# Performance work log

Hardware: AMD Instinct MI355X
Metric: run time of the kernel (lower is better)

## Reference

```python
import jax, jax.numpy as jnp
import numpy as np

REEIG_EPS = 1e-4  # SPDNet ReEig eigenvalue floor


def _semi_orth(key, ni, no):
    a = jax.random.normal(key, (ni, no), dtype=jnp.float32)
    q, _ = jnp.linalg.qr(a)  # columns orthonormal (ni >= no)
    return q[None]  # (1, ni, no)


def setup_inputs() -> dict:
    key = jax.random.key(0)
    ks = jax.random.split(key, 6)
    N, C, T, V = 256, 256, 64, 25
    x = jax.random.normal(ks[0], (N, C, T, V), dtype=jnp.float32)
    W1 = _semi_orth(ks[1], 25, 20)
    W2 = _semi_orth(ks[2], 20, 15)
    W3 = _semi_orth(ks[3], 15, 10)
    fc_w = jax.random.normal(ks[4], (64, 100), dtype=jnp.float32) * (1.0 / np.sqrt(100))
    fc_b = jax.random.normal(ks[5], (64,), dtype=jnp.float32) * 0.01
    return {"x": x, "W1": W1, "W2": W2, "W3": W3, "fc_w": fc_w, "fc_b": fc_b}


def _bimap(X, W):
    # X: (n, h, ni, ni), W: (h, ni, no) -> W^T X W : (n, h, no, no)
    return jnp.einsum('hji,nhjk,hkl->nhil', W, X, W)


def _reeig(X):
    w, u = jnp.linalg.eigh(X)
    w = jnp.maximum(w, REEIG_EPS)
    return jnp.einsum('...ij,...j,...kj->...ik', u, w, u)


def _logeig(X):
    w, u = jnp.linalg.eigh(X)
    return jnp.einsum('...ij,...j,...kj->...ik', u, jnp.log(w), u)


def reference(x, W1, W2, W3, fc_w, fc_b):
    N, C, T, V = x.shape
    xm = x.mean(axis=2)                      # (N, C, V): mean over time
    d = xm - xm.mean(axis=1, keepdims=True)  # center over channel samples
    cov = jnp.einsum('ncv,ncw->nvw', d, d) / (C - 1)  # (N, V, V), fused reduction
    cov = cov + jnp.float32(1e-8) * jnp.eye(V, dtype=x.dtype)
    X = cov[:, None, :, :]                   # (N, 1, V, V)
    X = _reeig(_bimap(X, W1))                # 25 -> 20
    X = _reeig(_bimap(X, W2))                # 20 -> 15
    X = _logeig(_reeig(_bimap(X, W3)))       # 15 -> 10, matrix log
    feat = X.reshape(N, -1)                  # (N, 100)
    return feat @ fc_w.T + fc_b              # (N, 64)
```

## Files before the change

### kernel.cpp

```cpp
#include <hip/hip_runtime.h>
#include <math.h>


__device__ __constant__ int d_pairs[9][5][2] = {
    {{9,0},{1,8},{2,7},{3,6},{4,5}},
    {{9,1},{2,0},{3,8},{4,7},{5,6}},
    {{9,2},{3,1},{4,0},{5,8},{6,7}},
    {{9,3},{4,2},{5,1},{6,0},{7,8}},
    {{9,4},{5,3},{6,2},{7,1},{8,0}},
    {{9,5},{6,4},{7,3},{8,2},{0,1}},
    {{9,6},{7,5},{8,4},{0,3},{1,2}},
    {{9,7},{8,6},{0,5},{1,4},{2,3}},
    {{9,8},{0,7},{1,6},{2,5},{3,4}},
};

__global__ __launch_bounds__(256) void topo_kernel(
    const float* __restrict__ x,
    const float* __restrict__ W1,
    const float* __restrict__ W2,
    const float* __restrict__ W3,
    const float* __restrict__ fcw,
    const float* __restrict__ fcb,
    float* __restrict__ out)
{
    __shared__ float s_xm[6400];
    __shared__ float s_mean[32];
    __shared__ float s_w1[500];
    __shared__ float s_w2[300];
    __shared__ float s_w3[152];
    __shared__ float s_t1[375];
    __shared__ float s_wc[250];
    __shared__ float s_E[2560];
    __shared__ float s_A[100];
    __shared__ float s_U[100];
    __shared__ float s_cp[10], s_cq[10];
    __shared__ int   s_ip[10], s_iq[10];
    __shared__ float s_lw[16];
    __shared__ float s_Y[100];
    __shared__ float s_fcw[100 * 65];

    const int tid = threadIdx.x;
    const int n = blockIdx.x;
    const float* xb = x + (size_t)n * (256 * 64 * 25);

    for (int g = tid; g < 6400; g += 256) {
        int o = g / 100, k = g - o * 100;
        s_fcw[k * 65 + o] = fcw[g];
    }
    for (int g = tid; g < 500; g += 256) s_w1[g] = W1[g];
    for (int g = tid; g < 300; g += 256) s_w2[g] = W2[g];
    if (tid < 150) s_w3[tid] = W3[tid];

    float acc[25];
    int   bidx[25];
#pragma unroll
    for (int k = 0; k < 25; ++k) {
        int o = tid + 256 * k;
        int c = o / 25, v = o - c * 25;
        bidx[k] = c * 1600 + v;
        acc[k] = 0.0f;
    }
#pragma unroll 4
    for (int t = 0; t < 64; ++t) {
#pragma unroll
        for (int k = 0; k < 25; ++k) {
            acc[k] += __builtin_nontemporal_load(&xb[bidx[k] + t * 25]);
        }
    }
#pragma unroll
    for (int k = 0; k < 25; ++k)
        s_xm[tid + 256 * k] = acc[k] * (1.0f / 64.0f);
    __syncthreads();

    for (int g = tid; g < 375; g += 256) {
        int i = g / 15, l = g - i * 15;
        float s = 0.0f;
#pragma unroll
        for (int j = 0; j < 20; ++j) s += s_w1[i * 20 + j] * s_w2[j * 15 + l];
        s_t1[g] = s;
    }
    if (tid < 25) {
        float s = 0.0f;
        for (int c = 0; c < 256; ++c) s += s_xm[c * 25 + tid];
        s_mean[tid] = s * (1.0f / 256.0f);
    }
    __syncthreads();

    for (int g = tid; g < 250; g += 256) {
        int i = g / 10, m = g - i * 10;
        float s = 0.0f;
#pragma unroll
        for (int l = 0; l < 15; ++l) s += s_t1[i * 15 + l] * s_w3[l * 10 + m];
        s_wc[g] = s;
    }
#pragma unroll
    for (int k = 0; k < 25; ++k) {
        int o = tid + 256 * k;
        int v = o - (o / 25) * 25;
        s_xm[o] = s_xm[o] - s_mean[v];
    }
    __syncthreads();

#pragma unroll
    for (int k = 0; k < 10; ++k) {
        int idx = tid + 256 * k;
        int c = idx / 10, i = idx - c * 10;
        float s = 0.0f;
#pragma unroll
        for (int v = 0; v < 25; ++v) s += s_xm[c * 25 + v] * s_wc[v * 10 + i];
        s_E[idx] = s;
    }
    __syncthreads();

    if (tid < 55) {
        int i = 0, rem = tid;
        while (rem >= 10 - i) { rem -= 10 - i; ++i; }
        int j = i + rem;
        float s = 0.0f;
        for (int c = 0; c < 256; ++c) s += s_E[c * 10 + i] * s_E[c * 10 + j];
        float wt = 0.0f;
#pragma unroll
        for (int v = 0; v < 25; ++v) wt += s_wc[v * 10 + i] * s_wc[v * 10 + j];
        float m = s * (1.0f / 255.0f) + 1e-8f * wt;
        s_A[i * 10 + j] = m;
        s_A[j * 10 + i] = m;
    }
    if (tid >= 64 && tid < 164) {
        int e = tid - 64;
        s_U[e] = ((e / 10) == (e % 10)) ? 1.0f : 0.0f;
    }
    __syncthreads();

    for (int sweep = 0; sweep < 8; ++sweep) {
        for (int r = 0; r < 9; ++r) {
            if (tid < 5) {
                int p = d_pairs[r][tid][0], q = d_pairs[r][tid][1];
                if (p > q) { int t = p; p = q; q = t; }
                float app = s_A[p * 10 + p];
                float aqq = s_A[q * 10 + q];
                float apq = s_A[p * 10 + q];
                float c, sn;
                if (fabsf(apq) < 1e-28f) {
                    c = 1.0f; sn = 0.0f;
                } else {
                    float tau = (aqq - app) / (2.0f * apq);
                    float tt = 1.0f / (fabsf(tau) + sqrtf(tau * tau + 1.0f));
                    if (tau < 0.0f) tt = -tt;
                    c = 1.0f / sqrtf(tt * tt + 1.0f);
                    sn = tt * c;
                }
                s_ip[p] = p; s_iq[p] = q; s_cp[p] = c;  s_cq[p] = -sn;
                s_ip[q] = p; s_iq[q] = q; s_cp[q] = sn; s_cq[q] = c;
            }
            __syncthreads();
            float newA = 0.0f, newU = 0.0f;
            if (tid < 100) {
                int i = tid / 10, j = tid - (tid / 10) * 10;
                float wip = s_cp[i], wiq = s_cq[i];
                float wjp = s_cp[j], wjq = s_cq[j];
                int pi_ = s_ip[i], qi_ = s_iq[i];
                int pj  = s_ip[j], qj  = s_iq[j];
                newA = wip * (wjp * s_A[pi_ * 10 + pj] + wjq * s_A[pi_ * 10 + qj])
                     + wiq * (wjp * s_A[qi_ * 10 + pj] + wjq * s_A[qi_ * 10 + qj]);
            } else if (tid < 200) {
                int e = tid - 100;
                int i = e / 10, j = e - (e / 10) * 10;
                int pj = s_ip[j], qj = s_iq[j];
                newU = s_cp[j] * s_U[i * 10 + pj] + s_cq[j] * s_U[i * 10 + qj];
            }
            __syncthreads();
            if (tid < 100)      s_A[tid] = newA;
            else if (tid < 200) s_U[tid - 100] = newU;
            __syncthreads();
        }
    }

    if (tid < 10) s_lw[tid] = logf(fmaxf(s_A[tid * 10 + tid], 1e-4f));
    __syncthreads();

    if (tid < 100) {
        int i = tid / 10, j = tid - (tid / 10) * 10;
        float s = 0.0f;
#pragma unroll
        for (int k = 0; k < 10; ++k) s += s_U[i * 10 + k] * s_lw[k] * s_U[j * 10 + k];
        s_Y[tid] = s;
    }
    __syncthreads();

    if (tid < 64) {
        float s = fcb[tid];
#pragma unroll 4
        for (int k = 0; k < 100; ++k) s += s_Y[k] * s_fcw[k * 65 + tid];
        out[(size_t)n * 64 + tid] = s;
    }
}

extern "C" void kernel_launch(void* const* d_in, const int* in_sizes, int n_in,
                              void* d_out, int out_size, void* d_ws, size_t ws_size,
                              hipStream_t stream) {
    const float* x   = (const float*)d_in[0];
    const float* W1  = (const float*)d_in[1];
    const float* W2  = (const float*)d_in[2];
    const float* W3  = (const float*)d_in[3];
    const float* fcw = (const float*)d_in[4];
    const float* fcb = (const float*)d_in[5];
    float* out = (float*)d_out;

    topo_kernel<<<256, 256, 0, stream>>>(x, W1, W2, W3, fcw, fcb, out);
}
```

Baseline: 634.2 us.

## Use 1024-thread blocks and float4 loads with shared atomics for time mean

```diff
diff --git a/kernel.cpp b/kernel.cpp
--- a/kernel.cpp
+++ b/kernel.cpp
@@ -14,7 +14,7 @@
     {{9,8},{0,7},{1,6},{2,5},{3,4}},
 };
 
-__global__ __launch_bounds__(256) void topo_kernel(
+__global__ __launch_bounds__(1024) void topo_kernel(
     const float* __restrict__ x,
     const float* __restrict__ W1,
     const float* __restrict__ W2,
@@ -43,36 +43,39 @@
     const int n = blockIdx.x;
     const float* xb = x + (size_t)n * (256 * 64 * 25);
 
-    for (int g = tid; g < 6400; g += 256) {
+    for (int g = tid; g < 6400; g += 1024) {
         int o = g / 100, k = g - o * 100;
         s_fcw[k * 65 + o] = fcw[g];
     }
-    for (int g = tid; g < 500; g += 256) s_w1[g] = W1[g];
-    for (int g = tid; g < 300; g += 256) s_w2[g] = W2[g];
+    for (int g = tid; g < 500; g += 1024) s_w1[g] = W1[g];
+    for (int g = tid; g < 300; g += 1024) s_w2[g] = W2[g];
     if (tid < 150) s_w3[tid] = W3[tid];
-
-    float acc[25];
-    int   bidx[25];
-#pragma unroll
-    for (int k = 0; k < 25; ++k) {
-        int o = tid + 256 * k;
-        int c = o / 25, v = o - c * 25;
-        bidx[k] = c * 1600 + v;
-        acc[k] = 0.0f;
-    }
-#pragma unroll 4
-    for (int t = 0; t < 64; ++t) {
-#pragma unroll
-        for (int k = 0; k < 25; ++k) {
-            acc[k] += __builtin_nontemporal_load(&xb[bidx[k] + t * 25]);
+    for (int g = tid; g < 6400; g += 1024) s_xm[g] = 0.0f;
+    __syncthreads();
+
+    {
+        const float4* xb4 = reinterpret_cast<const float4*>(xb);
+        for (int task = tid; task < 6400; task += 1024) {
+            int c = task / 25;
+            int m = task - c * 25;
+            const float4* p = xb4 + c * 400 + m;
+            float s0 = 0.0f, s1 = 0.0f, s2 = 0.0f, s3 = 0.0f;
+#pragma unroll
+            for (int k = 0; k < 16; ++k) {
+                float4 vv = p[25 * k];
+                s0 += vv.x; s1 += vv.y; s2 += vv.z; s3 += vv.w;
+            }
+            int v = (4 * m) % 25;
+            int base = c * 25;
+            atomicAdd(&s_xm[base + v], s0); v = (v + 1 == 25) ? 0 : v + 1;
+            atomicAdd(&s_xm[base + v], s1); v = (v + 1 == 25) ? 0 : v + 1;
+            atomicAdd(&s_xm[base + v], s2); v = (v + 1 == 25) ? 0 : v + 1;
+            atomicAdd(&s_xm[base + v], s3);
         }
     }
-#pragma unroll
-    for (int k = 0; k < 25; ++k)
-        s_xm[tid + 256 * k] = acc[k] * (1.0f / 64.0f);
-    __syncthreads();
-
-    for (int g = tid; g < 375; g += 256) {
+    __syncthreads();
+
+    for (int g = tid; g < 375; g += 1024) {
         int i = g / 15, l = g - i * 15;
         float s = 0.0f;
 #pragma unroll
@@ -82,29 +85,25 @@
     if (tid < 25) {
         float s = 0.0f;
         for (int c = 0; c < 256; ++c) s += s_xm[c * 25 + tid];
-        s_mean[tid] = s * (1.0f / 256.0f);
-    }
-    __syncthreads();
-
-    for (int g = tid; g < 250; g += 256) {
+        s_mean[tid] = s * (1.0f / (64.0f * 256.0f));
+    }
+    __syncthreads();
+
+    for (int g = tid; g < 250; g += 1024) {
         int i = g / 10, m = g - i * 10;
         float s = 0.0f;
 #pragma unroll
         for (int l = 0; l < 15; ++l) s += s_t1[i * 15 + l] * s_w3[l * 10 + m];
         s_wc[g] = s;
     }
-#pragma unroll
-    for (int k = 0; k < 25; ++k) {
-        int o = tid + 256 * k;
+    for (int o = tid; o < 6400; o += 1024) {
         int v = o - (o / 25) * 25;
-        s_xm[o] = s_xm[o] - s_mean[v];
-    }
-    __syncthreads();
-
-#pragma unroll
-    for (int k = 0; k < 10; ++k) {
-        int idx = tid + 256 * k;
-        int c = idx / 10, i = idx - c * 10;
+        s_xm[o] = s_xm[o] * (1.0f / 64.0f) - s_mean[v];
+    }
+    __syncthreads();
+
+    for (int idx = tid; idx < 2560; idx += 1024) {
+        int c = idx / 10, i = idx - (idx / 10) * 10;
         float s = 0.0f;
 #pragma unroll
         for (int v = 0; v < 25; ++v) s += s_xm[c * 25 + v] * s_wc[v * 10 + i];
@@ -206,5 +205,5 @@
     const float* fcb = (const float*)d_in[5];
     float* out = (float*)d_out;
 
-    topo_kernel<<<256, 256, 0, stream>>>(x, W1, W2, W3, fcw, fcb, out);
+    topo_kernel<<<256, 1024, 0, stream>>>(x, W1, W2, W3, fcw, fcb, out);
 }
```

Result: faster. 604.2 us (-4.7%).
